# Kernel tuning notes

Measured on AMD Instinct MI355X. Metric: run time of the kernel, lower is better.

## Reference

```python
import math
import jax, jax.numpy as jnp
import numpy as np

# cfg constants
IMG_W, IMG_H, CENTER_H = 800.0, 320.0, 160.0
NUM_OFFSETS = 72
ANGLE_THRES, RHO_THRES = 0.5, 0.5
CONF_THRES_O2O = 0.4
H_DIM, I_DIM, IOU_DIM = 64, 128, 1


def _lin(x, W, b):
    return x @ W + b


def setup_inputs() -> dict:
    B, N = 4, 512
    key = jax.random.key(0)
    ks = jax.random.split(key, 24)
    s = 0.05
    inp = {
        "batch_features": jax.random.normal(ks[0], (B, N, H_DIM), jnp.float32),
        "cls_pred": jax.random.uniform(ks[1], (B, N), jnp.float32),
        "anchor_id": jnp.tile(jnp.arange(N, dtype=jnp.int32), (B, 1)),
        "anchor_embeddings": 0.1 + 0.3 * jax.random.uniform(ks[2], (B, N, 2), jnp.float32),
        # cls_block
        "W_cls": s * jax.random.normal(ks[3], (H_DIM, H_DIM)), "b_cls": jnp.zeros((H_DIM,)),
        # LaneGNN
        "W_pos": s * jax.random.normal(ks[4], (2, I_DIM)), "b_pos": jnp.zeros((I_DIM,)),
        "W_in": s * jax.random.normal(ks[5], (H_DIM, I_DIM)), "b_in": jnp.zeros((I_DIM,)),
        "W_out": s * jax.random.normal(ks[6], (H_DIM, I_DIM)), "b_out": jnp.zeros((I_DIM,)),
        "W_e1": s * jax.random.normal(ks[7], (I_DIM, I_DIM)), "b_e1": jnp.zeros((I_DIM,)),
        "W_e2": s * jax.random.normal(ks[8], (I_DIM, IOU_DIM)), "b_e2": jnp.zeros((IOU_DIM,)),
        "W_n1": s * jax.random.normal(ks[9], (IOU_DIM, H_DIM)), "b_n1": jnp.zeros((H_DIM,)),
        "W_n2": s * jax.random.normal(ks[10], (H_DIM, H_DIM)), "b_n2": jnp.zeros((H_DIM,)),
        # cls_layer
        "W_head": s * jax.random.normal(ks[11], (H_DIM, 1)), "b_head": jnp.zeros((1,)),
    }
    return inp


def _get_nbr_mask(emb):
    angle = emb[..., 0] * math.pi
    rho = emb[..., 1] * IMG_W  # computed but unused due to original code's bug
    a = jnp.abs(angle[..., :, None] - angle[..., None, :])
    a = jnp.triu(a, k=1)
    a = a + jnp.swapaxes(a, -1, -2)
    # NOTE: faithful to original bug - rho matrix is rebuilt from the angle matrix
    r = jnp.triu(a, k=1)
    r = r + jnp.swapaxes(r, -1, -2)
    return (a < ANGLE_THRES) & (r < RHO_THRES)


def _get_sample_point(emb):
    B, N = emb.shape[0], emb.shape[1]
    e = emb.reshape(-1, 2)
    angle = e[:, 0] * math.pi
    rho = e[:, 1] * IMG_W
    lin = jnp.linspace(0.0, 1.0 - 1e-5, NUM_OFFSETS, dtype=jnp.float32)
    sample_car_y = (CENTER_H - lin * IMG_H)[:2]  # buffer keeps first 2
    x = -jnp.tan(angle)[:, None] * sample_car_y[None, :] + (rho / jnp.cos(angle))[:, None]
    return x.reshape(B, N, 2) / IMG_W


def reference(batch_features, cls_pred, anchor_id, anchor_embeddings,
              W_cls, b_cls, W_pos, b_pos, W_in, b_in, W_out, b_out,
              W_e1, b_e1, W_e2, b_e2, W_n1, b_n1, W_n2, b_n2, W_head, b_head):
    # suppression matrix (no-grad region in torch)
    nbr_masks = _get_nbr_mask(anchor_embeddings)
    cls_mat = cls_pred[..., :, None] - cls_pred[..., None, :]
    id_mat = (anchor_id[..., :, None] - anchor_id[..., None, :]).astype(jnp.float32)
    supress = ((cls_mat > 0) | ((cls_mat == 0) & (id_mat > 0))).astype(jnp.float32)
    supress = jnp.where(nbr_masks, supress, 0.0)
    pos_emb = _get_sample_point(anchor_embeddings)              # [B,N,2]
    pos_emb_mat = pos_emb[:, :, None, :] - pos_emb[:, None, :, :]  # [B,N,N,2]

    # cls_block
    feats = jax.nn.relu(_lin(batch_features, W_cls, b_cls))     # [B,N,H]

    # LaneGNN
    f_in = _lin(feats, W_in, b_in)    # [B,N,I]
    f_out = _lin(feats, W_out, b_out)  # [B,N,I]
    edge_emb = _lin(pos_emb_mat, W_pos, b_pos)  # [B,N,N,I]
    edge = f_in[:, :, None, :] - f_out[:, None, :, :] + edge_emb
    edge = _lin(jax.nn.gelu(_lin(edge, W_e1, b_e1), approximate=False), W_e2, b_e2)  # [B,N,N,iou]
    edge = edge * supress[..., None]
    node_max = jnp.max(edge, axis=1)  # [B,N,iou]
    node = jax.nn.relu(_lin(node_max, W_n1, b_n1))
    node = jax.nn.relu(_lin(node, W_n2, b_n2))

    logits = _lin(node, W_head, b_head)[..., 0]  # [B,N]
    logits = jnp.where(cls_pred < CONF_THRES_O2O, -1e6, logits)
    return jax.nn.sigmoid(logits)
```

## Files before the change

### kernel.cpp

```cpp
#include <hip/hip_runtime.h>
#include <math.h>

#define B  4
#define N  512
#define BN (B * N)
#define H  64
#define I  128

#define PI_F   3.14159265358979323846f
#define Y0_F   160.0f
#define Y1_F   155.4930028f
#define INV_W  (1.0f / 800.0f)

__device__ __forceinline__ float gelu_fast(float x) {
    float x2 = x * x;
    float t1 = __builtin_fmaf(x2, -2.0f * 0.0356774081f, -2.0f * 0.7978845608f);
    float e  = __expf(x * t1);
    return x * __builtin_amdgcn_rcpf(1.0f + e);
}

#define NPB 4

__global__ __launch_bounds__(256) void prep_kernel(
    const float* __restrict__ bf, const float* __restrict__ emb,
    const float* __restrict__ W_cls, const float* __restrict__ b_cls,
    const float* __restrict__ W_pos, const float* __restrict__ b_pos,
    const float* __restrict__ W_in,  const float* __restrict__ b_in,
    const float* __restrict__ W_out, const float* __restrict__ b_out,
    const float* __restrict__ W_e1,  const float* __restrict__ b_e1,
    float* __restrict__ Uo, float* __restrict__ Vo)
{
    __shared__ float sbf[NPB][64];
    __shared__ float sft[NPB][64];
    __shared__ float su[NPB][128];
    __shared__ float sv[NPB][128];
    __shared__ float sp[NPB][2];

    const int tid = threadIdx.x;
    const int node0 = blockIdx.x * NPB;

    {
        int nd = tid >> 6, d = tid & 63;
        sbf[nd][d] = bf[(node0 + nd) * 64 + d];
    }
    if (tid < NPB) {
        int g = node0 + tid;
        float ang = emb[g * 2] * PI_F;
        float t = tanf(ang);
        float rc = (emb[g * 2 + 1] * 800.0f) / cosf(ang);
        sp[tid][0] = (-t * Y0_F + rc) * INV_W;
        sp[tid][1] = (-t * Y1_F + rc) * INV_W;
    }
    __syncthreads();

    {
        int nd = tid >> 6, h = tid & 63;
        float a0 = 0.f, a1 = 0.f, a2 = 0.f, a3 = 0.f;
        #pragma unroll 4
        for (int d = 0; d < 64; d += 4) {
            a0 += sbf[nd][d + 0] * W_cls[(d + 0) * 64 + h];
            a1 += sbf[nd][d + 1] * W_cls[(d + 1) * 64 + h];
            a2 += sbf[nd][d + 2] * W_cls[(d + 2) * 64 + h];
            a3 += sbf[nd][d + 3] * W_cls[(d + 3) * 64 + h];
        }
        sft[nd][h] = fmaxf(b_cls[h] + ((a0 + a1) + (a2 + a3)), 0.0f);
    }
    __syncthreads();

    {
        int k = tid & 127, np = tid >> 7;
        int n0 = np * 2, n1 = n0 + 1;
        float wp0 = W_pos[k], wp1 = W_pos[128 + k];
        float pe0 = sp[n0][0] * wp0 + sp[n0][1] * wp1;
        float pe1 = sp[n1][0] * wp0 + sp[n1][1] * wp1;
        float bi = b_in[k] + b_pos[k], bo = b_out[k];
        float au0 = 0.f, av0 = 0.f, au1 = 0.f, av1 = 0.f;
        #pragma unroll 8
        for (int h = 0; h < 64; ++h) {
            float wi = W_in[h * 128 + k];
            float wo = W_out[h * 128 + k];
            float f0 = sft[n0][h], f1 = sft[n1][h];
            au0 += f0 * wi;  av0 += f0 * wo;
            au1 += f1 * wi;  av1 += f1 * wo;
        }
        su[n0][k] = au0 + bi + pe0;  sv[n0][k] = av0 + bo + pe0;
        su[n1][k] = au1 + bi + pe1;  sv[n1][k] = av1 + bo + pe1;
    }
    __syncthreads();

    {
        int k = tid & 127, np = tid >> 7;
        int n0 = np * 2, n1 = n0 + 1;
        float aU0 = 0.f, aV0 = 0.f, aU1 = 0.f, aV1 = 0.f;
        #pragma unroll 8
        for (int m = 0; m < 128; ++m) {
            float w = W_e1[m * 128 + k];
            aU0 += su[n0][m] * w;  aV0 += sv[n0][m] * w;
            aU1 += su[n1][m] * w;  aV1 += sv[n1][m] * w;
        }
        float be = b_e1[k];
        Uo[(node0 + n0) * 128 + k] = aU0 + be;
        Vo[(node0 + n0) * 128 + k] = aV0;
        Uo[(node0 + n1) * 128 + k] = aU1 + be;
        Vo[(node0 + n1) * 128 + k] = aV1;
    }
}

__global__ __launch_bounds__(256) void edge_kernel(
    const float* __restrict__ U, const float* __restrict__ V,
    const float* __restrict__ cls, const int* __restrict__ aid,
    const float* __restrict__ emb,
    const float* __restrict__ W_e2, const float* __restrict__ b_e2,
    const float* __restrict__ W_n1, const float* __restrict__ b_n1,
    const float* __restrict__ W_n2, const float* __restrict__ b_n2,
    const float* __restrict__ W_hd, const float* __restrict__ b_hd,
    float* __restrict__ out)
{
    const int col  = blockIdx.x;
    const int tid  = threadIdx.x;
    const int wave = tid >> 6;
    const int lane = tid & 63;

    __shared__ float Vs[128];
    __shared__ float w2s[128];
    __shared__ unsigned short lseg[4][128];
    __shared__ unsigned short list[512];
    __shared__ int wcnt[4];
    __shared__ float red[4];
    __shared__ float n1s[64];

    const float cls_j = cls[col];
    if (cls_j < 0.4f) {
        if (tid == 0) out[col] = 0.0f;
        return;
    }

    if (tid < 128) {
        Vs[tid]  = V[col * 128 + tid];
        w2s[tid] = W_e2[tid];
    }

    const int   rowbase = (col >> 9) << 9;
    const float ang_j   = emb[col * 2] * PI_F;
    const int   id_j    = aid[col];
    const float be2     = b_e2[0];

    int c = 0;
    #pragma unroll
    for (int rr = 0; rr < 2; ++rr) {
        int i  = wave * 128 + rr * 64 + lane;
        int gi = rowbase + i;
        float ci = cls[gi];
        bool m = (ci > cls_j) || (ci == cls_j && aid[gi] > id_j);
        if (m) m = fabsf(emb[gi * 2] * PI_F - ang_j) < 0.5f;
        unsigned long long bal = __ballot(m);
        int pre = __popcll(bal & ((1ull << lane) - 1ull));
        if (m) lseg[wave][c + pre] = (unsigned short)i;
        c += __popcll(bal);
    }
    if (lane == 0) wcnt[wave] = c;
    __syncthreads();

    const int c0 = wcnt[0], c1 = wcnt[1], c2 = wcnt[2], c3 = wcnt[3];
    const int o1 = c0, o2 = c0 + c1, o3 = o2 + c2;
    const int total = o3 + c3;
    for (int r = tid; r < c0; r += 256) list[r]      = lseg[0][r];
    for (int r = tid; r < c1; r += 256) list[o1 + r] = lseg[1][r];
    for (int r = tid; r < c2; r += 256) list[o2 + r] = lseg[2][r];
    for (int r = tid; r < c3; r += 256) list[o3 + r] = lseg[3][r];
    __syncthreads();

    float wm = 0.0f;
    const float4* V4 = (const float4*)Vs;
    const float4* g4 = (const float4*)w2s;
    for (int r = tid; r < total; r += 256) {
        int gi = rowbase + (int)list[r];
        const float4* Up = (const float4*)(U + gi * 128);
        float s0 = 0.f, s1 = 0.f, s2 = 0.f, s3 = 0.f;
        #pragma unroll 8
        for (int k4 = 0; k4 < 32; ++k4) {
            float4 u4 = Up[k4];
            float4 v4 = V4[k4];
            float4 w4 = g4[k4];
            s0 += gelu_fast(u4.x - v4.x) * w4.x;
            s1 += gelu_fast(u4.y - v4.y) * w4.y;
            s2 += gelu_fast(u4.z - v4.z) * w4.z;
            s3 += gelu_fast(u4.w - v4.w) * w4.w;
        }
        wm = fmaxf(wm, ((s0 + s1) + (s2 + s3)) + be2);
    }

    #pragma unroll
    for (int off = 32; off > 0; off >>= 1)
        wm = fmaxf(wm, __shfl_down(wm, off));
    if (lane == 0) red[wave] = wm;
    __syncthreads();

    if (wave == 0) {
        const float nm = fmaxf(fmaxf(red[0], red[1]), fmaxf(red[2], red[3]));
        n1s[lane] = fmaxf(nm * W_n1[lane] + b_n1[lane], 0.0f);
        float a = b_n2[lane];
        #pragma unroll 8
        for (int m2 = 0; m2 < 64; ++m2) a += n1s[m2] * W_n2[m2 * 64 + lane];
        a = fmaxf(a, 0.0f);
        float p = a * W_hd[lane];
        #pragma unroll
        for (int off = 32; off > 0; off >>= 1) p += __shfl_down(p, off);
        if (lane == 0) {
            float logit = p + b_hd[0];
            out[col] = 1.0f / (1.0f + expf(-logit));
        }
    }
}

extern "C" void kernel_launch(void* const* d_in, const int* in_sizes, int n_in,
                              void* d_out, int out_size, void* d_ws, size_t ws_size,
                              hipStream_t stream) {
    const float* bf    = (const float*)d_in[0];
    const float* cls   = (const float*)d_in[1];
    const int*   aid   = (const int*)  d_in[2];
    const float* emb   = (const float*)d_in[3];
    const float* W_cls = (const float*)d_in[4];
    const float* b_cls = (const float*)d_in[5];
    const float* W_pos = (const float*)d_in[6];
    const float* b_pos = (const float*)d_in[7];
    const float* W_in  = (const float*)d_in[8];
    const float* b_in  = (const float*)d_in[9];
    const float* W_out = (const float*)d_in[10];
    const float* b_out = (const float*)d_in[11];
    const float* W_e1  = (const float*)d_in[12];
    const float* b_e1  = (const float*)d_in[13];
    const float* W_e2  = (const float*)d_in[14];
    const float* b_e2  = (const float*)d_in[15];
    const float* W_n1  = (const float*)d_in[16];
    const float* b_n1  = (const float*)d_in[17];
    const float* W_n2  = (const float*)d_in[18];
    const float* b_n2  = (const float*)d_in[19];
    const float* W_hd  = (const float*)d_in[20];
    const float* b_hd  = (const float*)d_in[21];

    float* Uw = (float*)d_ws;
    float* Vw = Uw + BN * I;
    float* out = (float*)d_out;

    prep_kernel<<<BN / NPB, 256, 0, stream>>>(
        bf, emb, W_cls, b_cls, W_pos, b_pos, W_in, b_in, W_out, b_out,
        W_e1, b_e1, Uw, Vw);
    edge_kernel<<<BN, 256, 0, stream>>>(
        Uw, Vw, cls, aid, emb, W_e2, b_e2, W_n1, b_n1, W_n2, b_n2,
        W_hd, b_hd, out);
}
```

Measured before the change: 133.2 us.

## Split edge dot products across thread pairs and skip inactive nodes in prep

The edge kernel now gives each candidate row to two threads, each covering half of the 128-wide GELU dot product, and combines the halves with a lane xor shuffle. This doubles active threads when a column has fewer than 256 neighbours. The prep kernel now handles two nodes per block with one node per 128-thread half. It exits early when both nodes have confidence below the threshold, since their U and V rows are never read. The cost is extra shuffles and a smaller per-block work unit in prep, which reloads weights more often.

```diff
diff --git a/kernel.cpp b/kernel.cpp
--- a/kernel.cpp
+++ b/kernel.cpp
@@ -19,10 +19,9 @@
     return x * __builtin_amdgcn_rcpf(1.0f + e);
 }
 
-#define NPB 4
-
 __global__ __launch_bounds__(256) void prep_kernel(
-    const float* __restrict__ bf, const float* __restrict__ emb,
+    const float* __restrict__ bf, const float* __restrict__ cls,
+    const float* __restrict__ emb,
     const float* __restrict__ W_cls, const float* __restrict__ b_cls,
     const float* __restrict__ W_pos, const float* __restrict__ b_pos,
     const float* __restrict__ W_in,  const float* __restrict__ b_in,
@@ -30,20 +29,23 @@
     const float* __restrict__ W_e1,  const float* __restrict__ b_e1,
     float* __restrict__ Uo, float* __restrict__ Vo)
 {
-    __shared__ float sbf[NPB][64];
-    __shared__ float sft[NPB][64];
-    __shared__ float su[NPB][128];
-    __shared__ float sv[NPB][128];
-    __shared__ float sp[NPB][2];
-
-    const int tid = threadIdx.x;
-    const int node0 = blockIdx.x * NPB;
-
-    {
-        int nd = tid >> 6, d = tid & 63;
-        sbf[nd][d] = bf[(node0 + nd) * 64 + d];
-    }
-    if (tid < NPB) {
+    __shared__ float sft[2][64];
+    __shared__ float su[2][128];
+    __shared__ float sv[2][128];
+    __shared__ float sp[2][2];
+
+    const int tid   = threadIdx.x;
+    const int node0 = blockIdx.x * 2;
+    const int nd    = tid >> 7;
+    const int idx   = tid & 127;
+    const int gnode = node0 + nd;
+
+    const bool act0 = cls[node0]     >= 0.4f;
+    const bool act1 = cls[node0 + 1] >= 0.4f;
+    if (!act0 && !act1) return;
+    const bool act = nd ? act1 : act0;
+
+    if (tid < 2) {
         int g = node0 + tid;
         float ang = emb[g * 2] * PI_F;
         float t = tanf(ang);
@@ -51,58 +53,57 @@
         sp[tid][0] = (-t * Y0_F + rc) * INV_W;
         sp[tid][1] = (-t * Y1_F + rc) * INV_W;
     }
-    __syncthreads();
-
-    {
-        int nd = tid >> 6, h = tid & 63;
+
+    if (act) {
+        const int h  = idx >> 1;
+        const int kh = idx & 1;
+        const float* bfp = bf + gnode * 64 + kh * 32;
         float a0 = 0.f, a1 = 0.f, a2 = 0.f, a3 = 0.f;
-        #pragma unroll 4
-        for (int d = 0; d < 64; d += 4) {
-            a0 += sbf[nd][d + 0] * W_cls[(d + 0) * 64 + h];
-            a1 += sbf[nd][d + 1] * W_cls[(d + 1) * 64 + h];
-            a2 += sbf[nd][d + 2] * W_cls[(d + 2) * 64 + h];
-            a3 += sbf[nd][d + 3] * W_cls[(d + 3) * 64 + h];
-        }
-        sft[nd][h] = fmaxf(b_cls[h] + ((a0 + a1) + (a2 + a3)), 0.0f);
-    }
-    __syncthreads();
-
-    {
-        int k = tid & 127, np = tid >> 7;
-        int n0 = np * 2, n1 = n0 + 1;
-        float wp0 = W_pos[k], wp1 = W_pos[128 + k];
-        float pe0 = sp[n0][0] * wp0 + sp[n0][1] * wp1;
-        float pe1 = sp[n1][0] * wp0 + sp[n1][1] * wp1;
-        float bi = b_in[k] + b_pos[k], bo = b_out[k];
+        #pragma unroll
+        for (int d = 0; d < 32; d += 4) {
+            int dd = kh * 32 + d;
+            a0 += bfp[d + 0] * W_cls[(dd + 0) * 64 + h];
+            a1 += bfp[d + 1] * W_cls[(dd + 1) * 64 + h];
+            a2 += bfp[d + 2] * W_cls[(dd + 2) * 64 + h];
+            a3 += bfp[d + 3] * W_cls[(dd + 3) * 64 + h];
+        }
+        float a = (a0 + a1) + (a2 + a3);
+        a += __shfl_xor(a, 1);
+        if (kh == 0) sft[nd][h] = fmaxf(a + b_cls[h], 0.0f);
+    }
+    __syncthreads();
+
+    if (act) {
+        const int k = idx;
+        float pe = sp[nd][0] * W_pos[k] + sp[nd][1] * W_pos[128 + k];
         float au0 = 0.f, av0 = 0.f, au1 = 0.f, av1 = 0.f;
         #pragma unroll 8
-        for (int h = 0; h < 64; ++h) {
-            float wi = W_in[h * 128 + k];
-            float wo = W_out[h * 128 + k];
-            float f0 = sft[n0][h], f1 = sft[n1][h];
-            au0 += f0 * wi;  av0 += f0 * wo;
-            au1 += f1 * wi;  av1 += f1 * wo;
-        }
-        su[n0][k] = au0 + bi + pe0;  sv[n0][k] = av0 + bo + pe0;
-        su[n1][k] = au1 + bi + pe1;  sv[n1][k] = av1 + bo + pe1;
-    }
-    __syncthreads();
-
-    {
-        int k = tid & 127, np = tid >> 7;
-        int n0 = np * 2, n1 = n0 + 1;
+        for (int h2 = 0; h2 < 64; h2 += 2) {
+            float f0 = sft[nd][h2], f1 = sft[nd][h2 + 1];
+            au0 += f0 * W_in [h2 * 128 + k];
+            av0 += f0 * W_out[h2 * 128 + k];
+            au1 += f1 * W_in [(h2 + 1) * 128 + k];
+            av1 += f1 * W_out[(h2 + 1) * 128 + k];
+        }
+        su[nd][k] = (au0 + au1) + b_in[k] + b_pos[k] + pe;
+        sv[nd][k] = (av0 + av1) + b_out[k] + pe;
+    }
+    __syncthreads();
+
+    if (act) {
+        const int k = idx;
         float aU0 = 0.f, aV0 = 0.f, aU1 = 0.f, aV1 = 0.f;
         #pragma unroll 8
-        for (int m = 0; m < 128; ++m) {
-            float w = W_e1[m * 128 + k];
-            aU0 += su[n0][m] * w;  aV0 += sv[n0][m] * w;
-            aU1 += su[n1][m] * w;  aV1 += sv[n1][m] * w;
-        }
-        float be = b_e1[k];
-        Uo[(node0 + n0) * 128 + k] = aU0 + be;
-        Vo[(node0 + n0) * 128 + k] = aV0;
-        Uo[(node0 + n1) * 128 + k] = aU1 + be;
-        Vo[(node0 + n1) * 128 + k] = aV1;
+        for (int m = 0; m < 128; m += 2) {
+            float w0 = W_e1[m * 128 + k];
+            float w1 = W_e1[(m + 1) * 128 + k];
+            float s0 = su[nd][m], t0 = sv[nd][m];
+            float s1 = su[nd][m + 1], t1 = sv[nd][m + 1];
+            aU0 += s0 * w0;  aV0 += t0 * w0;
+            aU1 += s1 * w1;  aV1 += t1 * w1;
+        }
+        Uo[gnode * 128 + k] = (aU0 + aU1) + b_e1[k];
+        Vo[gnode * 128 + k] = (aV0 + aV1);
     }
 }
 
@@ -173,21 +174,27 @@
     float wm = 0.0f;
     const float4* V4 = (const float4*)Vs;
     const float4* g4 = (const float4*)w2s;
-    for (int r = tid; r < total; r += 256) {
+    const int nitems = 2 * total;
+    for (int q = tid; q < nitems; q += 256) {
+        int r = q >> 1, half = q & 1;
         int gi = rowbase + (int)list[r];
-        const float4* Up = (const float4*)(U + gi * 128);
+        const float4* Up = (const float4*)(U + gi * 128) + half * 16;
+        const float4* Vp = V4 + half * 16;
+        const float4* Wp = g4 + half * 16;
         float s0 = 0.f, s1 = 0.f, s2 = 0.f, s3 = 0.f;
-        #pragma unroll 8
-        for (int k4 = 0; k4 < 32; ++k4) {
+        #pragma unroll
+        for (int k4 = 0; k4 < 16; ++k4) {
             float4 u4 = Up[k4];
-            float4 v4 = V4[k4];
-            float4 w4 = g4[k4];
+            float4 v4 = Vp[k4];
+            float4 w4 = Wp[k4];
             s0 += gelu_fast(u4.x - v4.x) * w4.x;
             s1 += gelu_fast(u4.y - v4.y) * w4.y;
             s2 += gelu_fast(u4.z - v4.z) * w4.z;
             s3 += gelu_fast(u4.w - v4.w) * w4.w;
         }
-        wm = fmaxf(wm, ((s0 + s1) + (s2 + s3)) + be2);
+        float s = (s0 + s1) + (s2 + s3);
+        s += __shfl_xor(s, 1);
+        if (half == 0) wm = fmaxf(wm, s + be2);
     }
 
     #pragma unroll
@@ -243,8 +250,8 @@
     float* Vw = Uw + BN * I;
     float* out = (float*)d_out;
 
-    prep_kernel<<<BN / NPB, 256, 0, stream>>>(
-        bf, emb, W_cls, b_cls, W_pos, b_pos, W_in, b_in, W_out, b_out,
+    prep_kernel<<<BN / 2, 256, 0, stream>>>(
+        bf, cls, emb, W_cls, b_cls, W_pos, b_pos, W_in, b_in, W_out, b_out,
         W_e1, b_e1, Uw, Vw);
     edge_kernel<<<BN, 256, 0, stream>>>(
         Uw, Vw, cls, aid, emb, W_e2, b_e2, W_n1, b_n1, W_n2, b_n2,
```

Measured after the change: 161.4 us. +21.2%, slower.

## Use single-wave edge blocks and 8-node prep blocks

Applied to the files above, without the earlier changes.

The edge kernel drops from four waves to a single 64-lane wave per column. The neighbour list is now built with one wave's ballots, so the cross-wave segment merge, the block barriers and the shared reduction go away. The prep kernel processes 8 nodes per 512-thread block so each block reuses the weight loads across more nodes. The risk is lower per-column parallelism: each lane now evaluates more neighbour rows serially when the list is long, and there are fewer waves in flight to hide the U row loads.

```diff
diff --git a/kernel.cpp b/kernel.cpp
--- a/kernel.cpp
+++ b/kernel.cpp
@@ -19,9 +19,7 @@
     return x * __builtin_amdgcn_rcpf(1.0f + e);
 }
 
-#define NPB 4
-
-__global__ __launch_bounds__(256) void prep_kernel(
+__global__ __launch_bounds__(512) void prep_kernel(
     const float* __restrict__ bf, const float* __restrict__ emb,
     const float* __restrict__ W_cls, const float* __restrict__ b_cls,
     const float* __restrict__ W_pos, const float* __restrict__ b_pos,
@@ -30,20 +28,17 @@
     const float* __restrict__ W_e1,  const float* __restrict__ b_e1,
     float* __restrict__ Uo, float* __restrict__ Vo)
 {
-    __shared__ float sbf[NPB][64];
-    __shared__ float sft[NPB][64];
-    __shared__ float su[NPB][128];
-    __shared__ float sv[NPB][128];
-    __shared__ float sp[NPB][2];
-
-    const int tid = threadIdx.x;
-    const int node0 = blockIdx.x * NPB;
-
-    {
-        int nd = tid >> 6, d = tid & 63;
-        sbf[nd][d] = bf[(node0 + nd) * 64 + d];
-    }
-    if (tid < NPB) {
+    __shared__ float sbf[8][64];
+    __shared__ float sft[8][64];
+    __shared__ float su[8][128];
+    __shared__ float sv[8][128];
+    __shared__ float sp[8][2];
+
+    const int tid   = threadIdx.x;
+    const int node0 = blockIdx.x * 8;
+
+    sbf[tid >> 6][tid & 63] = bf[node0 * 64 + tid];
+    if (tid < 8) {
         int g = node0 + tid;
         float ang = emb[g * 2] * PI_F;
         float t = tanf(ang);
@@ -54,45 +49,43 @@
     __syncthreads();
 
     {
-        int nd = tid >> 6, h = tid & 63;
-        float a0 = 0.f, a1 = 0.f, a2 = 0.f, a3 = 0.f;
+        const int nd = tid >> 6, h = tid & 63;
+        float a0 = 0.f, a1 = 0.f;
+        #pragma unroll 8
+        for (int d = 0; d < 64; d += 2) {
+            a0 += sbf[nd][d]     * W_cls[d * 64 + h];
+            a1 += sbf[nd][d + 1] * W_cls[(d + 1) * 64 + h];
+        }
+        sft[nd][h] = fmaxf(a0 + a1 + b_cls[h], 0.0f);
+    }
+    __syncthreads();
+
+    {
+        const int k = tid & 127, ng = tid >> 7;
+        const int n0 = ng * 2, n1 = n0 + 1;
+        float au0 = 0.f, av0 = 0.f, au1 = 0.f, av1 = 0.f;
         #pragma unroll 4
-        for (int d = 0; d < 64; d += 4) {
-            a0 += sbf[nd][d + 0] * W_cls[(d + 0) * 64 + h];
-            a1 += sbf[nd][d + 1] * W_cls[(d + 1) * 64 + h];
-            a2 += sbf[nd][d + 2] * W_cls[(d + 2) * 64 + h];
-            a3 += sbf[nd][d + 3] * W_cls[(d + 3) * 64 + h];
-        }
-        sft[nd][h] = fmaxf(b_cls[h] + ((a0 + a1) + (a2 + a3)), 0.0f);
-    }
-    __syncthreads();
-
-    {
-        int k = tid & 127, np = tid >> 7;
-        int n0 = np * 2, n1 = n0 + 1;
+        for (int h = 0; h < 64; ++h) {
+            float wi = W_in [h * 128 + k];
+            float wo = W_out[h * 128 + k];
+            float f0 = sft[n0][h], f1 = sft[n1][h];
+            au0 += f0 * wi;  av0 += f0 * wo;
+            au1 += f1 * wi;  av1 += f1 * wo;
+        }
         float wp0 = W_pos[k], wp1 = W_pos[128 + k];
         float pe0 = sp[n0][0] * wp0 + sp[n0][1] * wp1;
         float pe1 = sp[n1][0] * wp0 + sp[n1][1] * wp1;
         float bi = b_in[k] + b_pos[k], bo = b_out[k];
-        float au0 = 0.f, av0 = 0.f, au1 = 0.f, av1 = 0.f;
-        #pragma unroll 8
-        for (int h = 0; h < 64; ++h) {
-            float wi = W_in[h * 128 + k];
-            float wo = W_out[h * 128 + k];
-            float f0 = sft[n0][h], f1 = sft[n1][h];
-            au0 += f0 * wi;  av0 += f0 * wo;
-            au1 += f1 * wi;  av1 += f1 * wo;
-        }
         su[n0][k] = au0 + bi + pe0;  sv[n0][k] = av0 + bo + pe0;
         su[n1][k] = au1 + bi + pe1;  sv[n1][k] = av1 + bo + pe1;
     }
     __syncthreads();
 
     {
-        int k = tid & 127, np = tid >> 7;
-        int n0 = np * 2, n1 = n0 + 1;
+        const int k = tid & 127, ng = tid >> 7;
+        const int n0 = ng * 2, n1 = n0 + 1;
         float aU0 = 0.f, aV0 = 0.f, aU1 = 0.f, aV1 = 0.f;
-        #pragma unroll 8
+        #pragma unroll 4
         for (int m = 0; m < 128; ++m) {
             float w = W_e1[m * 128 + k];
             aU0 += su[n0][m] * w;  aV0 += sv[n0][m] * w;
@@ -106,7 +99,7 @@
     }
 }
 
-__global__ __launch_bounds__(256) void edge_kernel(
+__global__ __launch_bounds__(64) void edge_kernel(
     const float* __restrict__ U, const float* __restrict__ V,
     const float* __restrict__ cls, const int* __restrict__ aid,
     const float* __restrict__ emb,
@@ -117,75 +110,62 @@
     float* __restrict__ out)
 {
     const int col  = blockIdx.x;
-    const int tid  = threadIdx.x;
-    const int wave = tid >> 6;
-    const int lane = tid & 63;
+    const int lane = threadIdx.x;
+
+    const float cls_j = cls[col];
+    if (cls_j < 0.4f) {
+        if (lane == 0) out[col] = 0.0f;
+        return;
+    }
 
     __shared__ float Vs[128];
     __shared__ float w2s[128];
-    __shared__ unsigned short lseg[4][128];
     __shared__ unsigned short list[512];
-    __shared__ int wcnt[4];
-    __shared__ float red[4];
     __shared__ float n1s[64];
 
-    const float cls_j = cls[col];
-    if (cls_j < 0.4f) {
-        if (tid == 0) out[col] = 0.0f;
-        return;
-    }
-
-    if (tid < 128) {
-        Vs[tid]  = V[col * 128 + tid];
-        w2s[tid] = W_e2[tid];
-    }
-
-    const int   rowbase = (col >> 9) << 9;
+    Vs[lane]       = V[col * 128 + lane];
+    Vs[lane + 64]  = V[col * 128 + 64 + lane];
+    w2s[lane]      = W_e2[lane];
+    w2s[lane + 64] = W_e2[64 + lane];
+
+    const int   rowbase = col & ~(N - 1);
     const float ang_j   = emb[col * 2] * PI_F;
     const int   id_j    = aid[col];
     const float be2     = b_e2[0];
 
-    int c = 0;
-    #pragma unroll
-    for (int rr = 0; rr < 2; ++rr) {
-        int i  = wave * 128 + rr * 64 + lane;
-        int gi = rowbase + i;
-        float ci = cls[gi];
-        bool m = (ci > cls_j) || (ci == cls_j && aid[gi] > id_j);
-        if (m) m = fabsf(emb[gi * 2] * PI_F - ang_j) < 0.5f;
+    float ci[8]; int ai[8]; float an[8];
+    #pragma unroll
+    for (int rr = 0; rr < 8; ++rr) {
+        int gi = rowbase + rr * 64 + lane;
+        ci[rr] = cls[gi];
+        ai[rr] = aid[gi];
+        an[rr] = emb[gi * 2];
+    }
+
+    int cnt = 0;
+    #pragma unroll
+    for (int rr = 0; rr < 8; ++rr) {
+        bool m = (ci[rr] > cls_j) || (ci[rr] == cls_j && ai[rr] > id_j);
+        m = m && (fabsf(an[rr] * PI_F - ang_j) < 0.5f);
         unsigned long long bal = __ballot(m);
         int pre = __popcll(bal & ((1ull << lane) - 1ull));
-        if (m) lseg[wave][c + pre] = (unsigned short)i;
-        c += __popcll(bal);
-    }
-    if (lane == 0) wcnt[wave] = c;
-    __syncthreads();
-
-    const int c0 = wcnt[0], c1 = wcnt[1], c2 = wcnt[2], c3 = wcnt[3];
-    const int o1 = c0, o2 = c0 + c1, o3 = o2 + c2;
-    const int total = o3 + c3;
-    for (int r = tid; r < c0; r += 256) list[r]      = lseg[0][r];
-    for (int r = tid; r < c1; r += 256) list[o1 + r] = lseg[1][r];
-    for (int r = tid; r < c2; r += 256) list[o2 + r] = lseg[2][r];
-    for (int r = tid; r < c3; r += 256) list[o3 + r] = lseg[3][r];
-    __syncthreads();
+        if (m) list[cnt + pre] = (unsigned short)(rr * 64 + lane);
+        cnt += __popcll(bal);
+    }
 
     float wm = 0.0f;
-    const float4* V4 = (const float4*)Vs;
-    const float4* g4 = (const float4*)w2s;
-    for (int r = tid; r < total; r += 256) {
+    for (int r = lane; r < cnt; r += 64) {
         int gi = rowbase + (int)list[r];
-        const float4* Up = (const float4*)(U + gi * 128);
+        const float4* Up = (const float4*)(U + (size_t)gi * 128);
         float s0 = 0.f, s1 = 0.f, s2 = 0.f, s3 = 0.f;
         #pragma unroll 8
         for (int k4 = 0; k4 < 32; ++k4) {
             float4 u4 = Up[k4];
-            float4 v4 = V4[k4];
-            float4 w4 = g4[k4];
-            s0 += gelu_fast(u4.x - v4.x) * w4.x;
-            s1 += gelu_fast(u4.y - v4.y) * w4.y;
-            s2 += gelu_fast(u4.z - v4.z) * w4.z;
-            s3 += gelu_fast(u4.w - v4.w) * w4.w;
+            int k = k4 * 4;
+            s0 += gelu_fast(u4.x - Vs[k + 0]) * w2s[k + 0];
+            s1 += gelu_fast(u4.y - Vs[k + 1]) * w2s[k + 1];
+            s2 += gelu_fast(u4.z - Vs[k + 2]) * w2s[k + 2];
+            s3 += gelu_fast(u4.w - Vs[k + 3]) * w2s[k + 3];
         }
         wm = fmaxf(wm, ((s0 + s1) + (s2 + s3)) + be2);
     }
@@ -193,23 +173,19 @@
     #pragma unroll
     for (int off = 32; off > 0; off >>= 1)
         wm = fmaxf(wm, __shfl_down(wm, off));
-    if (lane == 0) red[wave] = wm;
-    __syncthreads();
-
-    if (wave == 0) {
-        const float nm = fmaxf(fmaxf(red[0], red[1]), fmaxf(red[2], red[3]));
-        n1s[lane] = fmaxf(nm * W_n1[lane] + b_n1[lane], 0.0f);
-        float a = b_n2[lane];
-        #pragma unroll 8
-        for (int m2 = 0; m2 < 64; ++m2) a += n1s[m2] * W_n2[m2 * 64 + lane];
-        a = fmaxf(a, 0.0f);
-        float p = a * W_hd[lane];
-        #pragma unroll
-        for (int off = 32; off > 0; off >>= 1) p += __shfl_down(p, off);
-        if (lane == 0) {
-            float logit = p + b_hd[0];
-            out[col] = 1.0f / (1.0f + expf(-logit));
-        }
+    const float nm = __shfl(wm, 0);
+
+    n1s[lane] = fmaxf(nm * W_n1[lane] + b_n1[lane], 0.0f);
+    float a = b_n2[lane];
+    #pragma unroll 8
+    for (int m2 = 0; m2 < 64; ++m2) a += n1s[m2] * W_n2[m2 * 64 + lane];
+    a = fmaxf(a, 0.0f);
+    float p = a * W_hd[lane];
+    #pragma unroll
+    for (int off = 32; off > 0; off >>= 1) p += __shfl_down(p, off);
+    if (lane == 0) {
+        float logit = p + b_hd[0];
+        out[col] = 1.0f / (1.0f + expf(-logit));
     }
 }
 
@@ -243,10 +219,10 @@
     float* Vw = Uw + BN * I;
     float* out = (float*)d_out;
 
-    prep_kernel<<<BN / NPB, 256, 0, stream>>>(
+    prep_kernel<<<BN / 8, 512, 0, stream>>>(
         bf, emb, W_cls, b_cls, W_pos, b_pos, W_in, b_in, W_out, b_out,
         W_e1, b_e1, Uw, Vw);
-    edge_kernel<<<BN, 256, 0, stream>>>(
+    edge_kernel<<<BN, 64, 0, stream>>>(
         Uw, Vw, cls, aid, emb, W_e2, b_e2, W_n1, b_n1, W_n2, b_n2,
         W_hd, b_hd, out);
 }
```

New measurement: 149.0 us. +11.9%, slower.

## Process two output columns per edge-kernel block with a merged work list

Applied to the files above, without the earlier changes.

Each block of the edge kernel now handles two adjacent columns. Two waves build the neighbour list for each column, and the two lists are merged into one index space so all 256 threads share the edge work. This halves the block count and balances load when one column has few neighbours or is below the confidence threshold. In exchange, V and W_e2 are now read as scalar LDS loads instead of float4, each item needs a branch to pick its list, and the block keeps two sets of accumulators.

```diff
diff --git a/kernel.cpp b/kernel.cpp
--- a/kernel.cpp
+++ b/kernel.cpp
@@ -116,99 +116,125 @@
     const float* __restrict__ W_hd, const float* __restrict__ b_hd,
     float* __restrict__ out)
 {
-    const int col  = blockIdx.x;
     const int tid  = threadIdx.x;
     const int wave = tid >> 6;
     const int lane = tid & 63;
-
-    __shared__ float Vs[128];
+    const int col0 = blockIdx.x * 2;
+    const int half = wave >> 1;
+    const int wsub = wave & 1;
+
+    __shared__ float Vs[2][128];
     __shared__ float w2s[128];
-    __shared__ unsigned short lseg[4][128];
-    __shared__ unsigned short list[512];
+    __shared__ unsigned short lseg[4][256];
+    __shared__ unsigned short lists[2][512];
     __shared__ int wcnt[4];
-    __shared__ float red[4];
-    __shared__ float n1s[64];
-
-    const float cls_j = cls[col];
-    if (cls_j < 0.4f) {
-        if (tid == 0) out[col] = 0.0f;
+    __shared__ float redm[2][4];
+    __shared__ float n1s[2][64];
+
+    const float clsA = cls[col0];
+    const float clsB = cls[col0 + 1];
+    if (clsA < 0.4f && clsB < 0.4f) {
+        if (tid < 2) out[col0 + tid] = 0.0f;
         return;
     }
 
-    if (tid < 128) {
-        Vs[tid]  = V[col * 128 + tid];
-        w2s[tid] = W_e2[tid];
-    }
-
-    const int   rowbase = (col >> 9) << 9;
-    const float ang_j   = emb[col * 2] * PI_F;
-    const int   id_j    = aid[col];
+    const int   mycol  = col0 + half;
+    const float cls_j  = half ? clsB : clsA;
+    const bool  active = cls_j >= 0.4f;
+
+    if (tid < 128) w2s[tid] = W_e2[tid];
+    if (wsub == 0) {
+        Vs[half][lane]      = V[mycol * 128 + lane];
+        Vs[half][lane + 64] = V[mycol * 128 + 64 + lane];
+    }
+
+    const int   rowbase = col0 & ~(N - 1);
+    const float ang_j   = emb[mycol * 2] * PI_F;
+    const int   id_j    = aid[mycol];
     const float be2     = b_e2[0];
 
-    int c = 0;
+    float ci[4]; int ai[4]; float an[4];
     #pragma unroll
-    for (int rr = 0; rr < 2; ++rr) {
-        int i  = wave * 128 + rr * 64 + lane;
-        int gi = rowbase + i;
-        float ci = cls[gi];
-        bool m = (ci > cls_j) || (ci == cls_j && aid[gi] > id_j);
-        if (m) m = fabsf(emb[gi * 2] * PI_F - ang_j) < 0.5f;
+    for (int rr = 0; rr < 4; ++rr) {
+        int gi = rowbase + wsub * 256 + rr * 64 + lane;
+        ci[rr] = cls[gi];
+        ai[rr] = aid[gi];
+        an[rr] = emb[gi * 2];
+    }
+    int cnt = 0;
+    #pragma unroll
+    for (int rr = 0; rr < 4; ++rr) {
+        bool m = active &&
+                 ((ci[rr] > cls_j) || (ci[rr] == cls_j && ai[rr] > id_j)) &&
+                 (fabsf(an[rr] * PI_F - ang_j) < 0.5f);
         unsigned long long bal = __ballot(m);
         int pre = __popcll(bal & ((1ull << lane) - 1ull));
-        if (m) lseg[wave][c + pre] = (unsigned short)i;
-        c += __popcll(bal);
-    }
-    if (lane == 0) wcnt[wave] = c;
+        if (m) lseg[wave][cnt + pre] = (unsigned short)(wsub * 256 + rr * 64 + lane);
+        cnt += __popcll(bal);
+    }
+    if (lane == 0) wcnt[wave] = cnt;
     __syncthreads();
 
     const int c0 = wcnt[0], c1 = wcnt[1], c2 = wcnt[2], c3 = wcnt[3];
-    const int o1 = c0, o2 = c0 + c1, o3 = o2 + c2;
-    const int total = o3 + c3;
-    for (int r = tid; r < c0; r += 256) list[r]      = lseg[0][r];
-    for (int r = tid; r < c1; r += 256) list[o1 + r] = lseg[1][r];
-    for (int r = tid; r < c2; r += 256) list[o2 + r] = lseg[2][r];
-    for (int r = tid; r < c3; r += 256) list[o3 + r] = lseg[3][r];
-    __syncthreads();
-
-    float wm = 0.0f;
-    const float4* V4 = (const float4*)Vs;
-    const float4* g4 = (const float4*)w2s;
-    for (int r = tid; r < total; r += 256) {
-        int gi = rowbase + (int)list[r];
-        const float4* Up = (const float4*)(U + gi * 128);
+    const int totA = c0 + c1, totB = c2 + c3;
+    for (int r = tid; r < c0; r += 256) lists[0][r]      = lseg[0][r];
+    for (int r = tid; r < c1; r += 256) lists[0][c0 + r] = lseg[1][r];
+    for (int r = tid; r < c2; r += 256) lists[1][r]      = lseg[2][r];
+    for (int r = tid; r < c3; r += 256) lists[1][c2 + r] = lseg[3][r];
+    __syncthreads();
+
+    float wmA = 0.0f, wmB = 0.0f;
+    const int nitems = totA + totB;
+    for (int q = tid; q < nitems; q += 256) {
+        int h = (q >= totA) ? 1 : 0;
+        int r = h ? (q - totA) : q;
+        int gi = rowbase + (int)lists[h][r];
+        const float4* Up = (const float4*)(U + (size_t)gi * 128);
+        const float*  Vp = Vs[h];
         float s0 = 0.f, s1 = 0.f, s2 = 0.f, s3 = 0.f;
         #pragma unroll 8
         for (int k4 = 0; k4 < 32; ++k4) {
             float4 u4 = Up[k4];
-            float4 v4 = V4[k4];
-            float4 w4 = g4[k4];
-            s0 += gelu_fast(u4.x - v4.x) * w4.x;
-            s1 += gelu_fast(u4.y - v4.y) * w4.y;
-            s2 += gelu_fast(u4.z - v4.z) * w4.z;
-            s3 += gelu_fast(u4.w - v4.w) * w4.w;
-        }
-        wm = fmaxf(wm, ((s0 + s1) + (s2 + s3)) + be2);
+            int k = k4 * 4;
+            s0 += gelu_fast(u4.x - Vp[k + 0]) * w2s[k + 0];
+            s1 += gelu_fast(u4.y - Vp[k + 1]) * w2s[k + 1];
+            s2 += gelu_fast(u4.z - Vp[k + 2]) * w2s[k + 2];
+            s3 += gelu_fast(u4.w - Vp[k + 3]) * w2s[k + 3];
+        }
+        float s = ((s0 + s1) + (s2 + s3)) + be2;
+        if (h) wmB = fmaxf(wmB, s); else wmA = fmaxf(wmA, s);
     }
 
     #pragma unroll
-    for (int off = 32; off > 0; off >>= 1)
-        wm = fmaxf(wm, __shfl_down(wm, off));
-    if (lane == 0) red[wave] = wm;
-    __syncthreads();
-
-    if (wave == 0) {
-        const float nm = fmaxf(fmaxf(red[0], red[1]), fmaxf(red[2], red[3]));
-        n1s[lane] = fmaxf(nm * W_n1[lane] + b_n1[lane], 0.0f);
-        float a = b_n2[lane];
-        #pragma unroll 8
-        for (int m2 = 0; m2 < 64; ++m2) a += n1s[m2] * W_n2[m2 * 64 + lane];
-        a = fmaxf(a, 0.0f);
-        float p = a * W_hd[lane];
-        #pragma unroll
-        for (int off = 32; off > 0; off >>= 1) p += __shfl_down(p, off);
-        if (lane == 0) {
-            float logit = p + b_hd[0];
-            out[col] = 1.0f / (1.0f + expf(-logit));
+    for (int off = 32; off > 0; off >>= 1) {
+        wmA = fmaxf(wmA, __shfl_down(wmA, off));
+        wmB = fmaxf(wmB, __shfl_down(wmB, off));
+    }
+    if (lane == 0) { redm[0][wave] = wmA; redm[1][wave] = wmB; }
+    __syncthreads();
+
+    if (wave < 2) {
+        const int   h    = wave;
+        const int   colh = col0 + h;
+        const float cj   = h ? clsB : clsA;
+        if (cj >= 0.4f) {
+            const float nm = fmaxf(fmaxf(redm[h][0], redm[h][1]),
+                                   fmaxf(redm[h][2], redm[h][3]));
+            n1s[h][lane] = fmaxf(nm * W_n1[lane] + b_n1[lane], 0.0f);
+            float a = b_n2[lane];
+            #pragma unroll 8
+            for (int m2 = 0; m2 < 64; ++m2)
+                a += n1s[h][m2] * W_n2[m2 * 64 + lane];
+            a = fmaxf(a, 0.0f);
+            float p = a * W_hd[lane];
+            #pragma unroll
+            for (int off = 32; off > 0; off >>= 1) p += __shfl_down(p, off);
+            if (lane == 0) {
+                float logit = p + b_hd[0];
+                out[colh] = 1.0f / (1.0f + expf(-logit));
+            }
+        } else if (lane == 0) {
+            out[colh] = 0.0f;
         }
     }
 }
@@ -246,7 +272,7 @@
     prep_kernel<<<BN / NPB, 256, 0, stream>>>(
         bf, emb, W_cls, b_cls, W_pos, b_pos, W_in, b_in, W_out, b_out,
         W_e1, b_e1, Uw, Vw);
-    edge_kernel<<<BN, 256, 0, stream>>>(
+    edge_kernel<<<BN / 2, 256, 0, stream>>>(
         Uw, Vw, cls, aid, emb, W_e2, b_e2, W_n1, b_n1, W_n2, b_n2,
         W_hd, b_hd, out);
 }
```

New measurement: 136.3 us. +2.4%, slower.
